# Performance work log

Measured on AMD Instinct MI355X. Metric: run time of the kernel, lower is better.

The kernel has to match this reference:

```python
import jax, jax.numpy as jnp
import numpy as np

MINLENGTH = 600

def setup_inputs() -> dict:
    key = jax.random.key(0)
    # values in [0, 600) so bincount output length == minlength == 600
    x = jax.random.randint(key, (33554432,), 0, 600, dtype=jnp.int32)
    return {"x": x}

def reference(x) -> jnp.ndarray:
    # torch.ops.aten.bincount(x, minlength=600): histogram of non-negative ints.
    # Since all values < 600 by construction, output length is exactly 600.
    # segment_sum of ones == scatter-increment histogram.
    ones = jnp.ones_like(x, dtype=jnp.int32)
    counts = jax.ops.segment_sum(ones, x, num_segments=MINLENGTH)
    return counts
```

## Files before the change

kernel.cpp:

```cpp
#include <hip/hip_runtime.h>
#include <hip/hip_bf16.h>

#define NBINS 600
#define NCOPIES 16

__global__ __launch_bounds__(256) void bincount_part(
        const int* __restrict__ x, int n, int* __restrict__ part) {
    __shared__ int h[NBINS * NCOPIES];

    for (int i = threadIdx.x; i < NBINS * NCOPIES; i += 256) h[i] = 0;
    __syncthreads();

    const int c = threadIdx.x & (NCOPIES - 1);
    const int n4 = n >> 2;
    const int4* __restrict__ x4 = (const int4*)x;
    const int stride = gridDim.x * 256;
    int i = blockIdx.x * 256 + threadIdx.x;

    for (; i + stride < n4; i += 2 * stride) {
        int4 a = x4[i];
        int4 b = x4[i + stride];
        atomicAdd(&h[a.x * NCOPIES + c], 1);
        atomicAdd(&h[a.y * NCOPIES + c], 1);
        atomicAdd(&h[a.z * NCOPIES + c], 1);
        atomicAdd(&h[a.w * NCOPIES + c], 1);
        atomicAdd(&h[b.x * NCOPIES + c], 1);
        atomicAdd(&h[b.y * NCOPIES + c], 1);
        atomicAdd(&h[b.z * NCOPIES + c], 1);
        atomicAdd(&h[b.w * NCOPIES + c], 1);
    }
    if (i < n4) {
        int4 a = x4[i];
        atomicAdd(&h[a.x * NCOPIES + c], 1);
        atomicAdd(&h[a.y * NCOPIES + c], 1);
        atomicAdd(&h[a.z * NCOPIES + c], 1);
        atomicAdd(&h[a.w * NCOPIES + c], 1);
    }
    if (blockIdx.x == 0) {
        for (int t = (n4 << 2) + (int)threadIdx.x; t < n; t += 256)
            atomicAdd(&h[x[t] * NCOPIES + c], 1);
    }

    __syncthreads();

    for (int b = threadIdx.x; b < NBINS; b += 256) {
        int s = 0;
        #pragma unroll
        for (int j = 0; j < NCOPIES; ++j)
            s += h[b * NCOPIES + ((j + threadIdx.x) & (NCOPIES - 1))];
        part[blockIdx.x * NBINS + b] = s;
    }
}

__global__ __launch_bounds__(256) void bincount_reduce(
        const int* __restrict__ part, int nblocks, int* __restrict__ out) {
    __shared__ int red[256];
    const int bin = blockIdx.x;
    int s = 0;
    for (int b = threadIdx.x; b < nblocks; b += 256)
        s += part[b * NBINS + bin];
    red[threadIdx.x] = s;
    __syncthreads();
    for (int off = 128; off > 0; off >>= 1) {
        if (threadIdx.x < off) red[threadIdx.x] += red[threadIdx.x + off];
        __syncthreads();
    }
    if (threadIdx.x == 0) out[bin] = red[0];
}

extern "C" void kernel_launch(void* const* d_in, const int* in_sizes, int n_in,
                              void* d_out, int out_size, void* d_ws, size_t ws_size,
                              hipStream_t stream) {
    const int* x = (const int*)d_in[0];
    int* out = (int*)d_out;
    int* part = (int*)d_ws;
    const int n = in_sizes[0];

    int nblocks = 1024;
    while ((size_t)nblocks * NBINS * sizeof(int) > ws_size && nblocks > 64)
        nblocks >>= 1;

    bincount_part<<<nblocks, 256, 0, stream>>>(x, n, part);
    bincount_reduce<<<NBINS, 256, 0, stream>>>(part, nblocks, out);
}
```

Measured before the change: 189.3 us.

## Software-pipeline loads, widen histogram copies, and use wave-shuffle reduction

The partial-histogram kernel now uses 512-thread blocks and 32 private copies per bin, which spreads LDS atomic contention across more banks. When the input divides evenly, the main loop is software-pipelined: it prefetches the next four int4 loads before doing atomics on the current ones. The reduce kernel switches to a single 64-lane wavefront with shuffle-down reduction instead of a shared-memory tree. Costs are 76.8 KB of LDS per block, which limits occupancy, and a grid halved to 512 blocks.

```diff
diff --git a/kernel.cpp b/kernel.cpp
--- a/kernel.cpp
+++ b/kernel.cpp
@@ -2,48 +2,56 @@
 #include <hip/hip_bf16.h>
 
 #define NBINS 600
-#define NCOPIES 16
+#define NCOPIES 32
 
-__global__ __launch_bounds__(256) void bincount_part(
+#define ATOM4(v)                                   \
+    atomicAdd(&h[(v).x * NCOPIES + c], 1);         \
+    atomicAdd(&h[(v).y * NCOPIES + c], 1);         \
+    atomicAdd(&h[(v).z * NCOPIES + c], 1);         \
+    atomicAdd(&h[(v).w * NCOPIES + c], 1);
+
+__global__ __launch_bounds__(512) void bincount_part(
         const int* __restrict__ x, int n, int* __restrict__ part) {
     __shared__ int h[NBINS * NCOPIES];
 
-    for (int i = threadIdx.x; i < NBINS * NCOPIES; i += 256) h[i] = 0;
+    for (int i = threadIdx.x; i < NBINS * NCOPIES; i += 512) h[i] = 0;
     __syncthreads();
 
     const int c = threadIdx.x & (NCOPIES - 1);
     const int n4 = n >> 2;
     const int4* __restrict__ x4 = (const int4*)x;
-    const int stride = gridDim.x * 256;
-    int i = blockIdx.x * 256 + threadIdx.x;
+    const int nth = gridDim.x * 512;
+    const int base = blockIdx.x * 512 + threadIdx.x;
+    const int per = n4 / nth;
 
-    for (; i + stride < n4; i += 2 * stride) {
-        int4 a = x4[i];
-        int4 b = x4[i + stride];
-        atomicAdd(&h[a.x * NCOPIES + c], 1);
-        atomicAdd(&h[a.y * NCOPIES + c], 1);
-        atomicAdd(&h[a.z * NCOPIES + c], 1);
-        atomicAdd(&h[a.w * NCOPIES + c], 1);
-        atomicAdd(&h[b.x * NCOPIES + c], 1);
-        atomicAdd(&h[b.y * NCOPIES + c], 1);
-        atomicAdd(&h[b.z * NCOPIES + c], 1);
-        atomicAdd(&h[b.w * NCOPIES + c], 1);
-    }
-    if (i < n4) {
-        int4 a = x4[i];
-        atomicAdd(&h[a.x * NCOPIES + c], 1);
-        atomicAdd(&h[a.y * NCOPIES + c], 1);
-        atomicAdd(&h[a.z * NCOPIES + c], 1);
-        atomicAdd(&h[a.w * NCOPIES + c], 1);
+    if (per * nth == n4 && (per & 3) == 0) {
+        int4 v0 = x4[base];
+        int4 v1 = x4[base + nth];
+        int4 v2 = x4[base + 2 * nth];
+        int4 v3 = x4[base + 3 * nth];
+        for (int k = 4; k < per; k += 4) {
+            int4 p0 = x4[base + (k + 0) * nth];
+            int4 p1 = x4[base + (k + 1) * nth];
+            int4 p2 = x4[base + (k + 2) * nth];
+            int4 p3 = x4[base + (k + 3) * nth];
+            ATOM4(v0); ATOM4(v1); ATOM4(v2); ATOM4(v3);
+            v0 = p0; v1 = p1; v2 = p2; v3 = p3;
+        }
+        ATOM4(v0); ATOM4(v1); ATOM4(v2); ATOM4(v3);
+    } else {
+        for (int i = base; i < n4; i += nth) {
+            int4 v = x4[i];
+            ATOM4(v);
+        }
     }
     if (blockIdx.x == 0) {
-        for (int t = (n4 << 2) + (int)threadIdx.x; t < n; t += 256)
+        for (int t = (n4 << 2) + (int)threadIdx.x; t < n; t += 512)
             atomicAdd(&h[x[t] * NCOPIES + c], 1);
     }
 
     __syncthreads();
 
-    for (int b = threadIdx.x; b < NBINS; b += 256) {
+    for (int b = threadIdx.x; b < NBINS; b += 512) {
         int s = 0;
         #pragma unroll
         for (int j = 0; j < NCOPIES; ++j)
@@ -52,20 +60,17 @@
     }
 }
 
-__global__ __launch_bounds__(256) void bincount_reduce(
+__global__ __launch_bounds__(64) void bincount_reduce(
         const int* __restrict__ part, int nblocks, int* __restrict__ out) {
-    __shared__ int red[256];
     const int bin = blockIdx.x;
+    const int t = threadIdx.x;
     int s = 0;
-    for (int b = threadIdx.x; b < nblocks; b += 256)
+    for (int b = t; b < nblocks; b += 64)
         s += part[b * NBINS + bin];
-    red[threadIdx.x] = s;
-    __syncthreads();
-    for (int off = 128; off > 0; off >>= 1) {
-        if (threadIdx.x < off) red[threadIdx.x] += red[threadIdx.x + off];
-        __syncthreads();
-    }
-    if (threadIdx.x == 0) out[bin] = red[0];
+    #pragma unroll
+    for (int off = 32; off > 0; off >>= 1)
+        s += __shfl_down(s, off, 64);
+    if (t == 0) out[bin] = s;
 }
 
 extern "C" void kernel_launch(void* const* d_in, const int* in_sizes, int n_in,
@@ -76,10 +81,10 @@
     int* part = (int*)d_ws;
     const int n = in_sizes[0];
 
-    int nblocks = 1024;
+    int nblocks = 512;
     while ((size_t)nblocks * NBINS * sizeof(int) > ws_size && nblocks > 64)
         nblocks >>= 1;
 
-    bincount_part<<<nblocks, 256, 0, stream>>>(x, n, part);
-    bincount_reduce<<<NBINS, 256, 0, stream>>>(part, nblocks, out);
+    bincount_part<<<nblocks, 512, 0, stream>>>(x, n, part);
+    bincount_reduce<<<NBINS, 64, 0, stream>>>(part, nblocks, out);
 }
```

New measurement: 192.1 us (median of 2 runs). Within noise of the previous version (+1.5%).
